# Optimization experiments

Hardware: AMD Instinct MI355X
Metric: run time of the kernel (lower is better)

Reference implementation:

```python
import jax, jax.numpy as jnp
import numpy as np

B, IN, OUT, NW = 8192, 4096, 4096, 16
NH, ND2 = NW // 3, NW // 3          # 5 haar, 5 db2
ND4 = NW - NH - ND2                  # 6 db4

DB2_HI = jnp.array([-0.1294095225512604, -0.2241438680420134,
                    0.8365163037378079, -0.4829629131445341], dtype=jnp.float32)
DB4_HI = jnp.array([-0.0074578275060427, -0.0233534968567756, 0.0218081502370024,
                    0.1323683939878645, -0.0197721859913265, -0.4461007108737368,
                    0.5055922216746659, -0.1629171572809054], dtype=jnp.float32)


def setup_inputs() -> dict:
    key = jax.random.key(0)
    ks = jax.random.split(key, 4)
    x = jax.random.normal(ks[0], (B, IN), dtype=jnp.float32)
    # kaiming-normal fan_in linear init -> std = 1/sqrt(fan_in); biases zero
    lin_w = jax.random.normal(ks[1], (OUT, IN), dtype=jnp.float32) * (1.0 / np.sqrt(IN))
    lin_b = jnp.zeros((OUT,), jnp.float32)
    proj_w = jax.random.normal(ks[2], (NW, IN), dtype=jnp.float32) * (1.0 / np.sqrt(IN))
    proj_b = jnp.zeros((NW,), jnp.float32)
    # exact _init_parameters values for the 'mixed' case
    scales = jnp.concatenate([jnp.logspace(-0.5, 0.5, NH),
                              jnp.logspace(-0.3, 0.7, ND2),
                              jnp.logspace(-0.3, 0.7, ND4)]).astype(jnp.float32)
    translations = jnp.concatenate([jnp.linspace(-1.5, 1.5, NH),
                                    jnp.linspace(-1.5, 1.5, ND2),
                                    jnp.linspace(-1.5, 1.5, ND4)]).astype(jnp.float32)
    comb_w = jax.random.normal(ks[3], (OUT, NW), dtype=jnp.float32) * (1.0 / np.sqrt(NW))
    comb_b = jnp.zeros((OUT,), jnp.float32)
    ln_g = jnp.ones((OUT,), jnp.float32)
    ln_beta = jnp.zeros((OUT,), jnp.float32)
    return dict(x=x, lin_w=lin_w, lin_b=lin_b, proj_w=proj_w, proj_b=proj_b,
                scales=scales, translations=translations,
                comb_w=comb_w, comb_b=comb_b, ln_g=ln_g, ln_beta=ln_beta)


def _haar_mother(sx):
    # Haar mother wavelet: +1 on [0, 0.5), -1 on [0.5, 1)
    return (((sx >= 0.0) & (sx < 0.5)).astype(jnp.float32)
            - ((sx >= 0.5) & (sx < 1.0)).astype(jnp.float32))


def _db_feature(val, scale, trans, filt, max_shift, mult):
    # db*_wavelet_transform + simplified_transform (scalar per wavelet)
    scale_factor = jax.nn.sigmoid(scale) * 2.0
    shift = jnp.clip(jnp.round(trans * mult), 0, max_shift).astype(jnp.int32)
    f = jnp.roll(filt, shift) * scale_factor
    feat = jnp.mean(val * jnp.sin(f * 5.0))
    return feat / (jnp.sum(jnp.abs(f)) * 0.1)  # filter_sum always > 0 here


def reference(x, lin_w, lin_b, proj_w, proj_b, scales, translations,
              comb_w, comb_b, ln_g, ln_beta):
    direct = x @ lin_w.T + lin_b                 # [B, OUT]
    proj = x @ proj_w.T + proj_b                 # [B, NW]

    # Haar wavelets on first NH projected channels (elementwise, per batch)
    sx = (proj[:, :NH] - translations[:NH]) / scales[:NH]
    haar = _haar_mother(sx)                      # [B, NH]

    # Daubechies 'simplified_transform': mean of first min(4,B) batch entries per column
    vals = jnp.mean(proj[:4, :], axis=0)         # [NW]
    db2 = jax.vmap(lambda v, s, t: _db_feature(v, s, t, DB2_HI, 3, 4.0))(
        vals[NH:NH + ND2], scales[NH:NH + ND2], translations[NH:NH + ND2])
    db4 = jax.vmap(lambda v, s, t: _db_feature(v, s, t, DB4_HI, 7, 8.0))(
        vals[NH + ND2:], scales[NH + ND2:], translations[NH + ND2:])
    db = jnp.broadcast_to(jnp.concatenate([db2, db4])[None, :],
                          (x.shape[0], ND2 + ND4))  # [B, ND2+ND4]

    wave = jnp.concatenate([haar, db], axis=1)   # [B, NW]
    wave_path = wave @ comb_w.T + comb_b         # [B, OUT]

    y = direct + wave_path
    mu = jnp.mean(y, axis=-1, keepdims=True)
    var = jnp.mean((y - mu) ** 2, axis=-1, keepdims=True)
    return (y - mu) * jax.lax.rsqrt(var + 1e-5) * ln_g + ln_beta
```

## Files before the change

### kernel.cpp

```cpp
#include <hip/hip_runtime.h>
#include <hip/hip_bf16.h>
#include <stdint.h>

constexpr int BDIM = 8192;
constexpr int INDIM = 4096;
constexpr int OUTDIM = 4096;

typedef __attribute__((ext_vector_type(8))) short bf16x8;
typedef __attribute__((ext_vector_type(4))) float f32x4;

__device__ __forceinline__ uint16_t f2bf_rne(float f) {
  union { float f; uint32_t u; } v; v.f = f;
  uint32_t r = v.u + 0x7fffu + ((v.u >> 16) & 1u);
  return (uint16_t)(r >> 16);
}

__device__ __forceinline__ void gload_lds16(const void* g, void* l) {
  __builtin_amdgcn_global_load_lds(
      (const __attribute__((address_space(1))) void*)g,
      (__attribute__((address_space(3))) void*)l, 16, 0, 0);
}

__global__ __launch_bounds__(256) void k_conv_w(const float* __restrict__ w,
                                                uint16_t* __restrict__ wb) {
  const int n4 = (OUTDIM * INDIM) / 4;
  for (int i = blockIdx.x * 256 + threadIdx.x; i < n4; i += gridDim.x * 256) {
    float4 v = ((const float4*)w)[i];
    ushort4 o;
    o.x = f2bf_rne(v.x); o.y = f2bf_rne(v.y);
    o.z = f2bf_rne(v.z); o.w = f2bf_rne(v.w);
    ((ushort4*)wb)[i] = o;
  }
}

__global__ __launch_bounds__(256) void k_conv_x_haar(
    const float* __restrict__ x, const float* __restrict__ proj_w,
    const float* __restrict__ proj_b, const float* __restrict__ scales,
    const float* __restrict__ trans, uint16_t* __restrict__ xb,
    float* __restrict__ haar) {
  const int row = blockIdx.x;
  const int tid = threadIdx.x;
  const float4* xr = (const float4*)(x + (size_t)row * INDIM);
  ushort4* xbr = (ushort4*)(xb + (size_t)row * INDIM);
  float acc[5] = {0.f, 0.f, 0.f, 0.f, 0.f};
#pragma unroll
  for (int c = 0; c < 4; ++c) {
    int i4 = tid + c * 256;
    float4 v = xr[i4];
    ushort4 o;
    o.x = f2bf_rne(v.x); o.y = f2bf_rne(v.y);
    o.z = f2bf_rne(v.z); o.w = f2bf_rne(v.w);
    xbr[i4] = o;
#pragma unroll
    for (int j = 0; j < 5; ++j) {
      float4 p = ((const float4*)(proj_w + (size_t)j * INDIM))[i4];
      acc[j] += v.x * p.x + v.y * p.y + v.z * p.z + v.w * p.w;
    }
  }
  __shared__ float wred[4][5];
  const int lane = tid & 63, w = tid >> 6;
#pragma unroll
  for (int j = 0; j < 5; ++j) {
    float v = acc[j];
#pragma unroll
    for (int off = 32; off; off >>= 1) v += __shfl_down(v, off, 64);
    if (lane == 0) wred[w][j] = v;
  }
  __syncthreads();
  if (tid < 5) {
    float p = wred[0][tid] + wred[1][tid] + wred[2][tid] + wred[3][tid] + proj_b[tid];
    float sx = (p - trans[tid]) / scales[tid];
    float h = 0.f;
    if (sx >= 0.f && sx < 0.5f) h = 1.f;
    else if (sx >= 0.5f && sx < 1.f) h = -1.f;
    haar[(size_t)row * 5 + tid] = h;
  }
}

__global__ __launch_bounds__(256) void k_db_c(
    const float* __restrict__ x, const float* __restrict__ proj_w,
    const float* __restrict__ proj_b, const float* __restrict__ scales,
    const float* __restrict__ lin_b, const float* __restrict__ comb_w,
    const float* __restrict__ comb_b, float* __restrict__ cvec,
    float* __restrict__ W5) {
  __shared__ float wred[4][11];
  __shared__ float dbs[11];
  const int tid = threadIdx.x, lane = tid & 63, w = tid >> 6;
  float acc[11];
#pragma unroll
  for (int j = 0; j < 11; ++j) acc[j] = 0.f;
  for (int r = 0; r < 4; ++r) {
    const float4* xr = (const float4*)(x + (size_t)r * INDIM);
    for (int c = tid; c < INDIM / 4; c += 256) {
      float4 v = xr[c];
#pragma unroll
      for (int j = 0; j < 11; ++j) {
        float4 p = ((const float4*)(proj_w + (size_t)(j + 5) * INDIM))[c];
        acc[j] += v.x * p.x + v.y * p.y + v.z * p.z + v.w * p.w;
      }
    }
  }
#pragma unroll
  for (int j = 0; j < 11; ++j) {
    float v = acc[j];
#pragma unroll
    for (int off = 32; off; off >>= 1) v += __shfl_down(v, off, 64);
    if (lane == 0) wred[w][j] = v;
  }
  __syncthreads();
  if (tid == 0) {
    const float DB2[4] = {-0.1294095225512604f, -0.2241438680420134f,
                          0.8365163037378079f, -0.4829629131445341f};
    const float DB4[8] = {-0.0074578275060427f, -0.0233534968567756f,
                          0.0218081502370024f,  0.1323683939878645f,
                          -0.0197721859913265f, -0.4461007108737368f,
                          0.5055922216746659f,  -0.1629171572809054f};
    for (int j = 0; j < 11; ++j) {
      float sum = wred[0][j] + wred[1][j] + wred[2][j] + wred[3][j];
      float val = sum * 0.25f + proj_b[j + 5];
      float sc = scales[j + 5];
      float sf = 2.f / (1.f + expf(-sc));
      const float* filt = (j < 5) ? DB2 : DB4;
      int L = (j < 5) ? 4 : 8;
      float ssin = 0.f, sabs = 0.f;
      for (int i = 0; i < L; ++i) {
        float fi = filt[i] * sf;
        ssin += sinf(fi * 5.0f);
        sabs += fabsf(fi);
      }
      dbs[j] = val * (ssin / (float)L) / (sabs * 0.1f);
    }
  }
  __syncthreads();
  for (int o = tid; o < OUTDIM; o += 256) {
    const float* cw = comb_w + (size_t)o * 16;
    float cc = lin_b[o] + comb_b[o];
#pragma unroll
    for (int j = 0; j < 11; ++j) cc += dbs[j] * cw[5 + j];
    cvec[o] = cc;
#pragma unroll
    for (int j = 0; j < 5; ++j) W5[j * OUTDIM + o] = cw[j];
  }
}


#define BARX() __builtin_amdgcn_s_barrier()
#define LGKM0() do { asm volatile("s_waitcnt lgkmcnt(0)" ::: "memory"); \
                     __builtin_amdgcn_sched_barrier(0); } while (0)
#define VM6() asm volatile("s_waitcnt vmcnt(6)" ::: "memory")

#define STAGE_A(t, q) do { \
  const char* _s = aSrc + (size_t)(q) * 64 * 8192 + (size_t)((t) & 63) * 128; \
  char* _l = sA + ((t) & 1) * 32768 + (q) * 8192 + ldsStage; \
  gload_lds16(_s, _l); gload_lds16(_s + 128 * 8192, _l + 16384); } while (0)

#define STAGE_B(t, h) do { \
  const char* _s = bSrc + (size_t)(h) * 128 * 8192 + (size_t)((t) & 63) * 128; \
  char* _l = sB + ((t) & 1) * 32768 + (h) * 16384 + ldsStage; \
  gload_lds16(_s, _l); gload_lds16(_s + 64 * 8192, _l + 8192); } while (0)

#define RDA4(buf, mb) do { const char* _p = sA + (buf) * 32768; \
  _Pragma("unroll") for (int _m = 0; _m < 4; ++_m) { \
    ar[_m][0] = *(const bf16x8*)(_p + (aoff + ((mb) + _m) * 2048)); \
    ar[_m][1] = *(const bf16x8*)(_p + ((aoff ^ 64) + ((mb) + _m) * 2048)); } } while (0)

#define RDB2(buf, arr, nb) do { const char* _p = sB + (buf) * 32768; \
  _Pragma("unroll") for (int _n = 0; _n < 2; ++_n) { \
    arr[_n][0] = *(const bf16x8*)(_p + (boff + ((nb) + _n) * 2048)); \
    arr[_n][1] = *(const bf16x8*)(_p + ((boff ^ 64) + ((nb) + _n) * 2048)); } } while (0)

#define MF8(mb, arrB, nb) do { \
  __builtin_amdgcn_s_setprio(1); \
  _Pragma("unroll") for (int _m = 0; _m < 4; ++_m) \
  _Pragma("unroll") for (int _n = 0; _n < 2; ++_n) { \
    acc[(mb) + _m][(nb) + _n] = __builtin_amdgcn_mfma_f32_16x16x32_bf16( \
        ar[_m][0], arrB[_n][0], acc[(mb) + _m][(nb) + _n], 0, 0, 0); \
    acc[(mb) + _m][(nb) + _n] = __builtin_amdgcn_mfma_f32_16x16x32_bf16( \
        ar[_m][1], arrB[_n][1], acc[(mb) + _m][(nb) + _n], 0, 0, 0); } \
  __builtin_amdgcn_s_setprio(0); } while (0)

__global__ __launch_bounds__(512, 2) void k_gemm(const uint16_t* __restrict__ A,
                                                 const uint16_t* __restrict__ Bw,
                                                 float* __restrict__ C) {
  constexpr int K = INDIM;
  constexpr int N = OUTDIM;
  extern __shared__ char smem[];
  char* sA = smem;
  char* sB = smem + 65536;

  const int tid = threadIdx.x;
  const int wid = tid >> 6;
  const int lane = tid & 63;
  const int l15 = lane & 15;
  const int kh = lane >> 4;
  const int wm = wid >> 2;
  const int wn = wid & 3;

  const int nwg = gridDim.x;
  const int bid = blockIdx.x;
  const int wg = (bid & 7) * (nwg >> 3) + (bid >> 3);
  constexpr int NBN = N / 256;
  const int mblk = wg / NBN, nblk = wg % NBN;
  const size_t arow = (size_t)mblk * 256, brow = (size_t)nblk * 256;

  const int srow = tid >> 3;
  const int scol = ((tid & 7) * 16) ^ ((srow & 7) << 4);
  const char* aSrc = (const char*)A + (arow + srow) * 8192 + scol;
  const char* bSrc = (const char*)Bw + (brow + srow) * 8192 + scol;
  const int ldsStage = wid * 1024;

  const int col0 = (kh * 16) ^ ((l15 & 7) << 4);
  const int aoff = (wm * 128 + l15) * 128 + col0;
  const int boff = (wn * 64 + l15) * 128 + col0;

  f32x4 acc[8][4];
#pragma unroll
  for (int m = 0; m < 8; ++m)
#pragma unroll
    for (int n = 0; n < 4; ++n) acc[m][n] = (f32x4){0.f, 0.f, 0.f, 0.f};
  bf16x8 ar[4][2], b01[2][2], b23[2][2];

  STAGE_A(0, 0); STAGE_A(0, 1); STAGE_B(0, 0); STAGE_B(0, 1);
  STAGE_A(1, 0); STAGE_B(1, 0); STAGE_B(1, 1);
  VM6(); BARX();

  for (int it = 0; it < K / 128; ++it) {
    const int t1 = it * 2 + 1, t2 = it * 2 + 2, t3 = it * 2 + 3;
    RDA4(0, 0); RDB2(0, b01, 0);
    STAGE_A(t1, 1);
    BARX(); LGKM0(); MF8(0, b01, 0); BARX();
    RDB2(0, b23, 2);
    STAGE_A(t2, 0);
    BARX(); LGKM0(); MF8(0, b23, 2); BARX();
    RDA4(0, 4);
    STAGE_B(t2, 0);
    BARX(); LGKM0(); MF8(4, b01, 0); BARX();
    STAGE_B(t2, 1);
    BARX(); LGKM0(); MF8(4, b23, 2);
    VM6(); BARX();
    RDA4(1, 0); RDB2(1, b01, 0);
    STAGE_A(t2, 1);
    BARX(); LGKM0(); MF8(0, b01, 0); BARX();
    RDB2(1, b23, 2);
    STAGE_A(t3, 0);
    BARX(); LGKM0(); MF8(0, b23, 2); BARX();
    RDA4(1, 4);
    STAGE_B(t3, 0);
    BARX(); LGKM0(); MF8(4, b01, 0); BARX();
    STAGE_B(t3, 1);
    BARX(); LGKM0(); MF8(4, b23, 2);
    VM6(); BARX();
  }

  const size_t crow0 = arow + (size_t)wm * 128;
  const int ccol0 = (int)brow + wn * 64;
#pragma unroll
  for (int m = 0; m < 8; ++m) {
#pragma unroll
    for (int n = 0; n < 4; ++n) {
      float* cp = C + (crow0 + m * 16 + kh * 4) * N + ccol0 + n * 16 + l15;
#pragma unroll
      for (int j = 0; j < 4; ++j) cp[(size_t)j * N] = acc[m][n][j];
    }
  }
}

__global__ __launch_bounds__(256) void k_ln(
    float* __restrict__ y, const float* __restrict__ haar,
    const float* __restrict__ cvec, const float* __restrict__ W5,
    const float* __restrict__ g, const float* __restrict__ beta) {
  const int row = blockIdx.x;
  const int tid = threadIdx.x;
  const float h0 = haar[(size_t)row * 5 + 0];
  const float h1 = haar[(size_t)row * 5 + 1];
  const float h2 = haar[(size_t)row * 5 + 2];
  const float h3 = haar[(size_t)row * 5 + 3];
  const float h4 = haar[(size_t)row * 5 + 4];
  float4* yr = (float4*)(y + (size_t)row * OUTDIM);
  float4 vals[4];
  float s = 0.f, s2 = 0.f;
#pragma unroll
  for (int c = 0; c < 4; ++c) {
    int i4 = tid + c * 256;
    float4 d = yr[i4];
    float4 cv = ((const float4*)cvec)[i4];
    float4 w0 = ((const float4*)(W5 + 0 * OUTDIM))[i4];
    float4 w1 = ((const float4*)(W5 + 1 * OUTDIM))[i4];
    float4 w2 = ((const float4*)(W5 + 2 * OUTDIM))[i4];
    float4 w3 = ((const float4*)(W5 + 3 * OUTDIM))[i4];
    float4 w4 = ((const float4*)(W5 + 4 * OUTDIM))[i4];
    float4 t;
    t.x = d.x + cv.x + h0 * w0.x + h1 * w1.x + h2 * w2.x + h3 * w3.x + h4 * w4.x;
    t.y = d.y + cv.y + h0 * w0.y + h1 * w1.y + h2 * w2.y + h3 * w3.y + h4 * w4.y;
    t.z = d.z + cv.z + h0 * w0.z + h1 * w1.z + h2 * w2.z + h3 * w3.z + h4 * w4.z;
    t.w = d.w + cv.w + h0 * w0.w + h1 * w1.w + h2 * w2.w + h3 * w3.w + h4 * w4.w;
    vals[c] = t;
    s += t.x + t.y + t.z + t.w;
    s2 += t.x * t.x + t.y * t.y + t.z * t.z + t.w * t.w;
  }
  const int lane = tid & 63, w = tid >> 6;
#pragma unroll
  for (int off = 32; off; off >>= 1) {
    s += __shfl_down(s, off, 64);
    s2 += __shfl_down(s2, off, 64);
  }
  __shared__ float rs[4], rs2[4];
  __shared__ float smu, sinv;
  if (lane == 0) { rs[w] = s; rs2[w] = s2; }
  __syncthreads();
  if (tid == 0) {
    float S = rs[0] + rs[1] + rs[2] + rs[3];
    float S2 = rs2[0] + rs2[1] + rs2[2] + rs2[3];
    float mu = S / (float)OUTDIM;
    float var = S2 / (float)OUTDIM - mu * mu;
    smu = mu;
    sinv = rsqrtf(var + 1e-5f);
  }
  __syncthreads();
  const float mu = smu, inv = sinv;
#pragma unroll
  for (int c = 0; c < 4; ++c) {
    int i4 = tid + c * 256;
    float4 gg = ((const float4*)g)[i4];
    float4 bb = ((const float4*)beta)[i4];
    float4 t = vals[c];
    float4 o;
    o.x = (t.x - mu) * inv * gg.x + bb.x;
    o.y = (t.y - mu) * inv * gg.y + bb.y;
    o.z = (t.z - mu) * inv * gg.z + bb.z;
    o.w = (t.w - mu) * inv * gg.w + bb.w;
    yr[i4] = o;
  }
}

extern "C" void kernel_launch(void* const* d_in, const int* in_sizes, int n_in,
                              void* d_out, int out_size, void* d_ws, size_t ws_size,
                              hipStream_t stream) {
  const float* x      = (const float*)d_in[0];
  const float* lin_w  = (const float*)d_in[1];
  const float* lin_b  = (const float*)d_in[2];
  const float* proj_w = (const float*)d_in[3];
  const float* proj_b = (const float*)d_in[4];
  const float* scales = (const float*)d_in[5];
  const float* trans  = (const float*)d_in[6];
  const float* comb_w = (const float*)d_in[7];
  const float* comb_b = (const float*)d_in[8];
  const float* ln_g   = (const float*)d_in[9];
  const float* ln_b   = (const float*)d_in[10];
  float* out = (float*)d_out;

  char* ws = (char*)d_ws;
  uint16_t* xb  = (uint16_t*)ws;
  uint16_t* wb  = (uint16_t*)(ws + 67108864);
  float*    haar = (float*)(ws + 100663296);
  float*    cvec = (float*)(ws + 100827136);
  float*    W5   = (float*)(ws + 100843520);

  hipFuncSetAttribute((const void*)k_gemm,
                      hipFuncAttributeMaxDynamicSharedMemorySize, 131072);

  k_conv_w<<<2048, 256, 0, stream>>>(lin_w, wb);
  k_conv_x_haar<<<BDIM, 256, 0, stream>>>(x, proj_w, proj_b, scales, trans, xb, haar);
  k_db_c<<<1, 256, 0, stream>>>(x, proj_w, proj_b, scales, lin_b, comb_w, comb_b,
                                cvec, W5);
  k_gemm<<<(BDIM / 256) * (OUTDIM / 256), 512, 131072, stream>>>(xb, wb, out);
  k_ln<<<BDIM, 256, 0, stream>>>(out, haar, cvec, W5, ln_g, ln_b);
}
```

Baseline: 379.6 us.

## Software-pipeline LDS fragment reads one MFMA phase ahead with partial lgkmcnt waits

The GEMM main loop now issues the LDS reads for the next MFMA phase before the current phase's MFMAs. It adds a second A-fragment register set so reads and compute can overlap, and replaces full lgkmcnt(0) waits with partial counts. The vmcnt wait moves earlier to vmcnt(4), and sched barriers keep the instruction order fixed. This is meant to hide LDS read latency behind MFMA work, at the cost of more VGPRs under launch_bounds(512,2) and more fragile hand-tuned wait counts.

```diff
diff --git a/kernel.cpp b/kernel.cpp
--- a/kernel.cpp
+++ b/kernel.cpp
@@ -144,10 +144,11 @@
 }
 
 
+#define SBAR0() __builtin_amdgcn_sched_barrier(0)
 #define BARX() __builtin_amdgcn_s_barrier()
-#define LGKM0() do { asm volatile("s_waitcnt lgkmcnt(0)" ::: "memory"); \
+#define LGKM(n) do { asm volatile("s_waitcnt lgkmcnt(" #n ")" ::: "memory"); \
                      __builtin_amdgcn_sched_barrier(0); } while (0)
-#define VM6() asm volatile("s_waitcnt vmcnt(6)" ::: "memory")
+#define VMC(n) asm volatile("s_waitcnt vmcnt(" #n ")" ::: "memory")
 
 #define STAGE_A(t, q) do { \
   const char* _s = aSrc + (size_t)(q) * 64 * 8192 + (size_t)((t) & 63) * 128; \
@@ -159,24 +160,24 @@
   char* _l = sB + ((t) & 1) * 32768 + (h) * 16384 + ldsStage; \
   gload_lds16(_s, _l); gload_lds16(_s + 64 * 8192, _l + 8192); } while (0)
 
-#define RDA4(buf, mb) do { const char* _p = sA + (buf) * 32768; \
+#define RDA4(arr, buf, mb) do { const char* _p = sA + (buf) * 32768; \
   _Pragma("unroll") for (int _m = 0; _m < 4; ++_m) { \
-    ar[_m][0] = *(const bf16x8*)(_p + (aoff + ((mb) + _m) * 2048)); \
-    ar[_m][1] = *(const bf16x8*)(_p + ((aoff ^ 64) + ((mb) + _m) * 2048)); } } while (0)
+    arr[_m][0] = *(const bf16x8*)(_p + (aoff + ((mb) + _m) * 2048)); \
+    arr[_m][1] = *(const bf16x8*)(_p + ((aoff ^ 64) + ((mb) + _m) * 2048)); } } while (0)
 
 #define RDB2(buf, arr, nb) do { const char* _p = sB + (buf) * 32768; \
   _Pragma("unroll") for (int _n = 0; _n < 2; ++_n) { \
     arr[_n][0] = *(const bf16x8*)(_p + (boff + ((nb) + _n) * 2048)); \
     arr[_n][1] = *(const bf16x8*)(_p + ((boff ^ 64) + ((nb) + _n) * 2048)); } } while (0)
 
-#define MF8(mb, arrB, nb) do { \
+#define MF8(arrA, mb, arrB, nb) do { \
   __builtin_amdgcn_s_setprio(1); \
   _Pragma("unroll") for (int _m = 0; _m < 4; ++_m) \
   _Pragma("unroll") for (int _n = 0; _n < 2; ++_n) { \
     acc[(mb) + _m][(nb) + _n] = __builtin_amdgcn_mfma_f32_16x16x32_bf16( \
-        ar[_m][0], arrB[_n][0], acc[(mb) + _m][(nb) + _n], 0, 0, 0); \
+        arrA[_m][0], arrB[_n][0], acc[(mb) + _m][(nb) + _n], 0, 0, 0); \
     acc[(mb) + _m][(nb) + _n] = __builtin_amdgcn_mfma_f32_16x16x32_bf16( \
-        ar[_m][1], arrB[_n][1], acc[(mb) + _m][(nb) + _n], 0, 0, 0); } \
+        arrA[_m][1], arrB[_n][1], acc[(mb) + _m][(nb) + _n], 0, 0, 0); } \
   __builtin_amdgcn_s_setprio(0); } while (0)
 
 __global__ __launch_bounds__(512, 2) void k_gemm(const uint16_t* __restrict__ A,
@@ -218,38 +219,47 @@
   for (int m = 0; m < 8; ++m)
 #pragma unroll
     for (int n = 0; n < 4; ++n) acc[m][n] = (f32x4){0.f, 0.f, 0.f, 0.f};
-  bf16x8 ar[4][2], b01[2][2], b23[2][2];
+  bf16x8 ar[4][2], ar2[4][2], b01[2][2], b23[2][2];
 
   STAGE_A(0, 0); STAGE_A(0, 1); STAGE_B(0, 0); STAGE_B(0, 1);
   STAGE_A(1, 0); STAGE_B(1, 0); STAGE_B(1, 1);
-  VM6(); BARX();
+  VMC(6); BARX();
+  RDA4(ar, 0, 0); RDB2(0, b01, 0);
 
   for (int it = 0; it < K / 128; ++it) {
     const int t1 = it * 2 + 1, t2 = it * 2 + 2, t3 = it * 2 + 3;
-    RDA4(0, 0); RDB2(0, b01, 0);
+    SBAR0();
+    RDB2(0, b23, 2);
     STAGE_A(t1, 1);
-    BARX(); LGKM0(); MF8(0, b01, 0); BARX();
-    RDB2(0, b23, 2);
+    BARX(); LGKM(4); MF8(ar, 0, b01, 0); BARX();
+    SBAR0();
+    RDA4(ar2, 0, 4);
     STAGE_A(t2, 0);
-    BARX(); LGKM0(); MF8(0, b23, 2); BARX();
-    RDA4(0, 4);
+    BARX(); LGKM(8); MF8(ar, 0, b23, 2); BARX();
+    SBAR0();
     STAGE_B(t2, 0);
-    BARX(); LGKM0(); MF8(4, b01, 0); BARX();
+    BARX(); LGKM(0); MF8(ar2, 4, b01, 0);
+    VMC(4); BARX();
+    SBAR0();
+    RDA4(ar, 1, 0); RDB2(1, b01, 0);
     STAGE_B(t2, 1);
-    BARX(); LGKM0(); MF8(4, b23, 2);
-    VM6(); BARX();
-    RDA4(1, 0); RDB2(1, b01, 0);
+    BARX(); LGKM(12); MF8(ar2, 4, b23, 2); BARX();
+    SBAR0();
+    RDB2(1, b23, 2);
     STAGE_A(t2, 1);
-    BARX(); LGKM0(); MF8(0, b01, 0); BARX();
-    RDB2(1, b23, 2);
+    BARX(); LGKM(4); MF8(ar, 0, b01, 0); BARX();
+    SBAR0();
+    RDA4(ar2, 1, 4);
     STAGE_A(t3, 0);
-    BARX(); LGKM0(); MF8(0, b23, 2); BARX();
-    RDA4(1, 4);
+    BARX(); LGKM(8); MF8(ar, 0, b23, 2); BARX();
+    SBAR0();
     STAGE_B(t3, 0);
-    BARX(); LGKM0(); MF8(4, b01, 0); BARX();
+    BARX(); LGKM(0); MF8(ar2, 4, b01, 0);
+    VMC(4); BARX();
+    SBAR0();
+    RDA4(ar, 0, 0); RDB2(0, b01, 0);
     STAGE_B(t3, 1);
-    BARX(); LGKM0(); MF8(4, b23, 2);
-    VM6(); BARX();
+    BARX(); LGKM(12); MF8(ar2, 4, b23, 2); BARX();
   }
 
   const size_t crow0 = arow + (size_t)wm * 128;
```

Result: slower. 391.5 us (+3.1%).
